# Kernel tuning notes

Measured on AMD Instinct MI355X. Metric: run time of the kernel, lower is better.

Reference implementation:

```python
import jax, jax.numpy as jnp
import numpy as np

D_MODEL = 1024
NUM_HEADS = 16
D_K = D_MODEL // NUM_HEADS
ROPE_THETA = 10000.0


def apply_rope(x, positions):
    # x: (b, h, s, d_k), positions: (b, s) int
    half = D_K // 2
    inv_freq = ROPE_THETA ** (-jnp.arange(half, dtype=jnp.float32) * 2.0 / D_K)  # (half,)
    angles = positions[:, None, :, None].astype(jnp.float32) * inv_freq  # (b,1,s,half)
    cos, sin = jnp.cos(angles), jnp.sin(angles)
    x_even = x[..., 0::2]
    x_odd = x[..., 1::2]
    r_even = x_even * cos - x_odd * sin
    r_odd = x_even * sin + x_odd * cos
    # re-interleave
    out = jnp.stack([r_even, r_odd], axis=-1).reshape(x.shape)
    return out


def setup_inputs() -> dict:
    key = jax.random.key(0)
    k1, k2, k3, k4, k5 = jax.random.split(key, 5)
    b, s = 2, 2048
    scale = 1.0 / np.sqrt(D_MODEL)
    x = jax.random.normal(k1, (b, s, D_MODEL), dtype=jnp.float32)
    w_q = jax.random.normal(k2, (D_MODEL, D_MODEL), dtype=jnp.float32) * scale
    w_k = jax.random.normal(k3, (D_MODEL, D_MODEL), dtype=jnp.float32) * scale
    w_v = jax.random.normal(k4, (D_MODEL, D_MODEL), dtype=jnp.float32) * scale
    w_o = jax.random.normal(k5, (D_MODEL, D_MODEL), dtype=jnp.float32) * scale
    token_positions = jnp.broadcast_to(jnp.arange(s, dtype=jnp.int64 if jax.config.jax_enable_x64 else jnp.int32), (b, s))
    return {"x": x, "w_q": w_q, "w_k": w_k, "w_v": w_v, "w_o": w_o,
            "token_positions": token_positions}


def reference(x, w_q, w_k, w_v, w_o, token_positions):
    b, s, _ = x.shape
    # QKV projections: w_* are (h*d_k, d_model); y = x @ w^T
    def proj(w):
        y = jnp.einsum('bsd,ed->bse', x, w)  # (b,s,h*d_k)
        return y.reshape(b, s, NUM_HEADS, D_K).transpose(0, 2, 1, 3)  # (b,h,s,d_k)
    Q, K, V = proj(w_q), proj(w_k), proj(w_v)
    Q = apply_rope(Q, token_positions)
    K = apply_rope(K, token_positions)
    scores = jnp.einsum('bhqd,bhkd->bhqk', Q, K) / jnp.sqrt(jnp.float32(D_K))
    causal = jnp.tril(jnp.ones((s, s), dtype=bool))
    scores = jnp.where(causal[None, None], scores, -jnp.inf)
    attn = jax.nn.softmax(scores, axis=-1)
    out = jnp.einsum('bhqk,bhkd->bhqd', attn, V)  # (b,h,s,d_v)
    out = out.transpose(0, 2, 1, 3).reshape(b, s, NUM_HEADS * D_K)
    return jnp.einsum('bse,de->bsd', out, w_o)
```

## Files before the change

### kernel.cpp

```cpp
#include <hip/hip_runtime.h>

#define B_ 2
#define S_ 2048
#define DM 1024
#define NH 16
#define DK 64

using bf16x8  = __attribute__((ext_vector_type(8)))  short;
using f32x4   = __attribute__((ext_vector_type(4)))  float;

__device__ __forceinline__ float bf2f(short v){
  unsigned u = ((unsigned)(unsigned short)v) << 16;
  union { unsigned u; float f; } c; c.u = u; return c.f;
}
__device__ __forceinline__ short f2bf(float f){
  union { float f; unsigned u; } c; c.f = f;
  unsigned u = c.u + 0x7FFFu + ((c.u >> 16) & 1u);
  return (short)(u >> 16);
}
__device__ __forceinline__ unsigned packbf(float lo, float hi){
  union { float f; unsigned u; } a, b; a.f = lo; b.f = hi;
  return __builtin_amdgcn_perm(b.u, a.u, 0x07060302u);
}
__device__ __forceinline__ void gload16(const void* g, void* l){
  __builtin_amdgcn_global_load_lds(
    (const __attribute__((address_space(1))) unsigned*)g,
    (__attribute__((address_space(3))) unsigned*)l, 16, 0, 0);
}

__global__ void rope_table(const int* __restrict__ pos, float* __restrict__ tab){
  int idx = blockIdx.x * blockDim.x + threadIdx.x;
  if (idx >= B_ * S_ * 32) return;
  int j = idx & 31, bs = idx >> 5;
  float p = (float)pos[bs];
  float inv = powf(10000.0f, -(float)(2 * j) / 64.0f);
  float ang = p * inv;
  tab[(size_t)bs * 64 + j]      = cosf(ang);
  tab[(size_t)bs * 64 + 32 + j] = sinf(ang);
}

__global__ void cast_all(const float* __restrict__ x, const float* __restrict__ wq,
                         const float* __restrict__ wk, const float* __restrict__ wv,
                         const float* __restrict__ wo,
                         short* __restrict__ xb, short* __restrict__ wqkv,
                         short* __restrict__ wob){
  int i = blockIdx.x * blockDim.x + threadIdx.x;
  const float4* src; short4* dst;
  if (i < (1 << 20)){
    src = (const float4*)x + i; dst = (short4*)xb + i;
  } else {
    int j = i - (1 << 20);
    int seg = j >> 18, off = j & ((1 << 18) - 1);
    const float* sp = seg == 0 ? wq : seg == 1 ? wk : seg == 2 ? wv : wo;
    short* dp = seg < 3 ? wqkv + ((size_t)seg << 20) : wob;
    src = (const float4*)sp + off; dst = (short4*)dp + off;
  }
  float4 v = *src;
  short4 o; o.x = f2bf(v.x); o.y = f2bf(v.y); o.z = f2bf(v.z); o.w = f2bf(v.w);
  *dst = o;
}

__launch_bounds__(512)
__global__ void gemm_qkv(const short* __restrict__ A, const short* __restrict__ Bm,
                         const float* __restrict__ tab,
                         short* __restrict__ Qr, short* __restrict__ Kr,
                         short* __restrict__ Vq, int K){
  __shared__ short As[128 * 32];
  __shared__ short Bs[128 * 32];
  const int tid = threadIdx.x;
  const int l = tid & 63, w = tid >> 6;
  const int lr = l & 15, lg = l >> 4;
  const int wr = w >> 2, wc = w & 3;
  const int nwg = gridDim.x * gridDim.y;
  const int wg  = blockIdx.y * gridDim.x + blockIdx.x;
  const int sw  = (wg & 7) * (nwg >> 3) + (wg >> 3);
  const int bn  = sw % gridDim.x, bm = sw / gridDim.x;
  const short* Ab = A + (size_t)bm * 128 * K;
  const short* Bb = Bm + (size_t)bn * 128 * K;
  f32x4 acc[4][2];
  #pragma unroll
  for (int m = 0; m < 4; ++m)
    #pragma unroll
    for (int n = 0; n < 2; ++n) acc[m][n] = (f32x4){0.f, 0.f, 0.f, 0.f};
  const int r0 = tid >> 2, q4 = tid & 3;
  for (int kt = 0; kt < K; kt += 32){
    gload16(Ab + (size_t)r0 * K + kt + q4 * 8, As + tid * 8);
    gload16(Bb + (size_t)r0 * K + kt + q4 * 8, Bs + tid * 8);
    __syncthreads();
    bf16x8 a[4], bfr[2];
    #pragma unroll
    for (int m = 0; m < 4; ++m)
      a[m] = *(const bf16x8*)(As + (wr * 64 + m * 16 + lr) * 32 + lg * 8);
    #pragma unroll
    for (int n = 0; n < 2; ++n)
      bfr[n] = *(const bf16x8*)(Bs + (wc * 32 + n * 16 + lr) * 32 + lg * 8);
    #pragma unroll
    for (int m = 0; m < 4; ++m)
      #pragma unroll
      for (int n = 0; n < 2; ++n)
        acc[m][n] = __builtin_amdgcn_mfma_f32_16x16x32_bf16(a[m], bfr[n], acc[m][n], 0, 0, 0);
    __syncthreads();
  }
  #pragma unroll
  for (int m = 0; m < 4; ++m)
    #pragma unroll
    for (int n = 0; n < 2; ++n){
      const int col = bn * 128 + wc * 32 + n * 16 + lr;
      const int which = col >> 10;
      #pragma unroll
      for (int j = 0; j < 4; ++j){
        const int row = bm * 128 + wr * 64 + m * 16 + lg * 4 + j;
        float v = acc[m][n][j];
        if (which == 2){
          Vq[(size_t)row * 1024 + (col - 2048)] = f2bf(v);
        } else {
          const int d  = col & 63;
          const int dp = d >> 1;
          const float c = tab[(size_t)row * 64 + dp];
          const float s = tab[(size_t)row * 64 + 32 + dp];
          const float p = __shfl_xor(v, 1);
          float r = v * c + p * ((d & 1) ? s : -s);
          if (which == 0) r *= 0.125f;
          short* dst = which ? Kr : Qr;
          const int b = row >> 11, si = row & 2047;
          const int h = (col >> 6) & 15;
          dst[(((size_t)(b * NH + h)) * S_ + si) * DK + d] = f2bf(r);
        }
      }
    }
}

template<typename OutT>
__launch_bounds__(512)
__global__ void gemm_bt8(const short* __restrict__ A, const short* __restrict__ Bm,
                         OutT* __restrict__ C, int M, int N, int K){
  __shared__ short As[128 * 32];
  __shared__ short Bs[128 * 32];
  const int tid = threadIdx.x;
  const int l = tid & 63, w = tid >> 6;
  const int lr = l & 15, lg = l >> 4;
  const int wr = w >> 2, wc = w & 3;
  const int nwg = gridDim.x * gridDim.y;
  const int wg  = blockIdx.y * gridDim.x + blockIdx.x;
  const int sw  = (wg & 7) * (nwg >> 3) + (wg >> 3);
  const int bn  = sw % gridDim.x, bm = sw / gridDim.x;
  const short* Ab = A + (size_t)bm * 128 * K;
  const short* Bb = Bm + (size_t)bn * 128 * K;
  f32x4 acc[4][2];
  #pragma unroll
  for (int m = 0; m < 4; ++m)
    #pragma unroll
    for (int n = 0; n < 2; ++n) acc[m][n] = (f32x4){0.f, 0.f, 0.f, 0.f};
  const int r0 = tid >> 2, q4 = tid & 3;
  for (int kt = 0; kt < K; kt += 32){
    gload16(Ab + (size_t)r0 * K + kt + q4 * 8, As + tid * 8);
    gload16(Bb + (size_t)r0 * K + kt + q4 * 8, Bs + tid * 8);
    __syncthreads();
    bf16x8 a[4], bfr[2];
    #pragma unroll
    for (int m = 0; m < 4; ++m)
      a[m] = *(const bf16x8*)(As + (wr * 64 + m * 16 + lr) * 32 + lg * 8);
    #pragma unroll
    for (int n = 0; n < 2; ++n)
      bfr[n] = *(const bf16x8*)(Bs + (wc * 32 + n * 16 + lr) * 32 + lg * 8);
    #pragma unroll
    for (int m = 0; m < 4; ++m)
      #pragma unroll
      for (int n = 0; n < 2; ++n)
        acc[m][n] = __builtin_amdgcn_mfma_f32_16x16x32_bf16(a[m], bfr[n], acc[m][n], 0, 0, 0);
    __syncthreads();
  }
  #pragma unroll
  for (int m = 0; m < 4; ++m)
    #pragma unroll
    for (int n = 0; n < 2; ++n)
      #pragma unroll
      for (int j = 0; j < 4; ++j){
        int row = bm * 128 + wr * 64 + m * 16 + lg * 4 + j;
        int col = bn * 128 + wc * 32 + n * 16 + lr;
        float v = acc[m][n][j];
        if constexpr (__is_same(OutT, short)) C[(size_t)row * N + col] = f2bf(v);
        else                                  C[(size_t)row * N + col] = v;
      }
}

__global__ void vtrans(const short* __restrict__ Vq, short* __restrict__ Vt){
  __shared__ short t[64][72];
  const int tid = threadIdx.x;
  const int st = blockIdx.x, bh = blockIdx.y;
  const int b = bh >> 4, h = bh & 15;
  #pragma unroll
  for (int i = 0; i < 2; ++i){
    int c = tid + 256 * i;
    int sl = c >> 3, d8 = c & 7;
    const short* src = Vq + ((size_t)b * S_ + st * 64 + sl) * 1024 + h * 64 + d8 * 8;
    *(bf16x8*)(&t[sl][d8 * 8]) = *(const bf16x8*)src;
  }
  __syncthreads();
  #pragma unroll
  for (int i = 0; i < 2; ++i){
    int c = tid + 256 * i;
    int dl = c >> 3, s8 = c & 7;
    bf16x8 v;
    #pragma unroll
    for (int jj = 0; jj < 8; ++jj) v[jj] = t[s8 * 8 + jj][dl];
    short* dst = Vt + ((size_t)bh * DK + dl) * S_ + st * 64 + s8 * 8;
    *(bf16x8*)dst = v;
  }
}

__device__ __forceinline__ void attn_tile_step(
    const bf16x8 qa0, const bf16x8 qa1,
    f32x4 (&acc)[4], float& mrow, float& lsum,
    const short* Ks, const short* Vs, unsigned* pw,
    int diagmask, int lr, int lg, int wl){
  float sv[4][4];
  #pragma unroll
  for (int n = 0; n < 4; ++n){
    const int R = n * 16 + lr;
    const int c0 = lg ^ (R & 7);
    bf16x8 k0 = *(const bf16x8*)(Ks + R * 64 + c0 * 8);
    bf16x8 k1 = *(const bf16x8*)(Ks + R * 64 + (c0 ^ 4) * 8);
    f32x4 z = (f32x4){0.f, 0.f, 0.f, 0.f};
    z = __builtin_amdgcn_mfma_f32_16x16x32_bf16(k0, qa0, z, 0, 0, 0);
    z = __builtin_amdgcn_mfma_f32_16x16x32_bf16(k1, qa1, z, 0, 0, 0);
    #pragma unroll
    for (int j = 0; j < 4; ++j) sv[n][j] = z[j];
  }
  if (diagmask){
    const int qloc = wl * 16 + lr;
    #pragma unroll
    for (int n = 0; n < 4; ++n)
      #pragma unroll
      for (int j = 0; j < 4; ++j)
        if (n * 16 + lg * 4 + j > qloc) sv[n][j] = -1e30f;
  }
  float lm = sv[0][0];
  #pragma unroll
  for (int n = 0; n < 4; ++n)
    #pragma unroll
    for (int j = 0; j < 4; ++j) lm = fmaxf(lm, sv[n][j]);
  lm = fmaxf(lm, __shfl_xor(lm, 16));
  lm = fmaxf(lm, __shfl_xor(lm, 32));
  if (!__all(lm <= mrow + 8.f)){
    float mnew = fmaxf(mrow, lm);
    float corr = __expf(mrow - mnew);
    mrow = mnew;
    lsum *= corr;
    float cb[4];
    #pragma unroll
    for (int j = 0; j < 4; ++j) cb[j] = __shfl(corr, lg * 4 + j);
    #pragma unroll
    for (int n = 0; n < 4; ++n)
      #pragma unroll
      for (int j = 0; j < 4; ++j) acc[n][j] *= cb[j];
  }
  float psum = 0.f;
  #pragma unroll
  for (int n = 0; n < 4; ++n)
    #pragma unroll
    for (int j = 0; j < 4; ++j){
      float p = __expf(sv[n][j] - mrow);
      sv[n][j] = p; psum += p;
    }
  psum += __shfl_xor(psum, 16);
  psum += __shfl_xor(psum, 32);
  lsum += psum;
  const int swz = (lr & 7) << 2;
  #pragma unroll
  for (int n = 0; n < 4; ++n){
    pw[lr * 32 + ((n * 8 + lg * 2 + 0) ^ swz)] = packbf(sv[n][0], sv[n][1]);
    pw[lr * 32 + ((n * 8 + lg * 2 + 1) ^ swz)] = packbf(sv[n][2], sv[n][3]);
  }
  bf16x8 pa0 = *(const bf16x8*)(pw + lr * 32 + ((lg * 4) ^ swz));
  bf16x8 pa1 = *(const bf16x8*)(pw + lr * 32 + ((16 + lg * 4) ^ swz));
  #pragma unroll
  for (int n = 0; n < 4; ++n){
    const int R = n * 16 + lr;
    const int c0 = lg ^ (R & 7);
    bf16x8 v0 = *(const bf16x8*)(Vs + R * 64 + c0 * 8);
    bf16x8 v1 = *(const bf16x8*)(Vs + R * 64 + (c0 ^ 4) * 8);
    acc[n] = __builtin_amdgcn_mfma_f32_16x16x32_bf16(pa0, v0, acc[n], 0, 0, 0);
    acc[n] = __builtin_amdgcn_mfma_f32_16x16x32_bf16(pa1, v1, acc[n], 0, 0, 0);
  }
}

__launch_bounds__(512)
__global__ void attn_kernel(const short* __restrict__ Qr, const short* __restrict__ Kr,
                            const short* __restrict__ Vt, short* __restrict__ AO){
  __shared__ short Ks[2][64 * 64];
  __shared__ short Vs[2][64 * 64];
  __shared__ unsigned Pw[8][16 * 32];
  const int tid = threadIdx.x;
  const int l = tid & 63, w = tid >> 6;
  const int lr = l & 15, lg = l >> 4;
  const int wl = w & 3, wgp = w >> 2;
  const int qp = blockIdx.x, h = blockIdx.y, b = blockIdx.z;
  const int t0 = qp, t1 = 31 - qp;
  const int myqt = wgp ? t0 : t1;
  const int bh = b * NH + h;
  const short* Qp = Qr + (size_t)bh * S_ * DK;
  const short* Kp = Kr + (size_t)bh * S_ * DK;
  const short* Vp = Vt + (size_t)bh * DK * S_;

  bf16x8 qa0, qa1;
  {
    const short* q0 = Qp + (size_t)(myqt * 64 + wl * 16 + lr) * DK + lg * 8;
    qa0 = *(const bf16x8*)q0; qa1 = *(const bf16x8*)(q0 + 32);
  }
  f32x4 acc[4];
  float ms = -1e30f, ls = 0.f;
  #pragma unroll
  for (int n = 0; n < 4; ++n) acc[n] = (f32x4){0.f, 0.f, 0.f, 0.f};
  unsigned* pw = &Pw[w][0];
  const int r0 = tid >> 3, q8 = tid & 7;
  const int sq8 = q8 ^ (r0 & 7);

  gload16(Kp + (size_t)r0 * DK + sq8 * 8, &Ks[0][tid * 8]);
  gload16(Vp + (size_t)r0 * S_ + sq8 * 8, &Vs[0][tid * 8]);
  int cur = 0;
  for (int kt = 0; kt <= t1; ++kt){
    __syncthreads();
    if (kt < t1){
      gload16(Kp + (size_t)((kt + 1) * 64 + r0) * DK + sq8 * 8, &Ks[cur ^ 1][tid * 8]);
      gload16(Vp + (size_t)r0 * S_ + (kt + 1) * 64 + sq8 * 8,   &Vs[cur ^ 1][tid * 8]);
    }
    if (kt <= myqt)
      attn_tile_step(qa0, qa1, acc, ms, ls, Ks[cur], Vs[cur], pw, kt == myqt, lr, lg, wl);
    cur ^= 1;
  }
  const float li = 1.f / ls;
  #pragma unroll
  for (int j = 0; j < 4; ++j){
    const float d0 = __shfl(li, lg * 4 + j);
    #pragma unroll
    for (int n = 0; n < 4; ++n){
      int e = h * 64 + n * 16 + lr;
      int r = myqt * 64 + wl * 16 + lg * 4 + j;
      AO[((size_t)b * S_ + r) * DM + e] = f2bf(acc[n][j] * d0);
    }
  }
}

extern "C" void kernel_launch(void* const* d_in, const int* in_sizes, int n_in,
                              void* d_out, int out_size, void* d_ws, size_t ws_size,
                              hipStream_t stream){
  const float* x  = (const float*)d_in[0];
  const float* wq = (const float*)d_in[1];
  const float* wk = (const float*)d_in[2];
  const float* wv = (const float*)d_in[3];
  const float* wo = (const float*)d_in[4];
  const int*  pos = (const int*)d_in[5];

  char* ws = (char*)d_ws;
  short* xb   = (short*)(ws + 0);
  short* wqkv = (short*)(ws + ((size_t)8  << 20));
  short* wob  = (short*)(ws + ((size_t)14 << 20));
  short* Vq   = (short*)(ws + ((size_t)16 << 20));
  short* Qr   = (short*)(ws + ((size_t)40 << 20));
  short* Kr   = (short*)(ws + ((size_t)48 << 20));
  short* Vt   = (short*)(ws + ((size_t)56 << 20));
  float* tab  = (float*)(ws + ((size_t)64 << 20));
  short* AO   = xb;
  float* out  = (float*)d_out;

  rope_table<<<dim3((B_ * S_ * 32 + 255) / 256), dim3(256), 0, stream>>>(pos, tab);
  cast_all<<<dim3(8192), dim3(256), 0, stream>>>(x, wq, wk, wv, wo, xb, wqkv, wob);
  gemm_qkv<<<dim3(24, 32), dim3(512), 0, stream>>>(xb, wqkv, tab, Qr, Kr, Vq, 1024);
  vtrans<<<dim3(32, 32), dim3(256), 0, stream>>>(Vq, Vt);
  attn_kernel<<<dim3(16, NH, B_), dim3(512), 0, stream>>>(Qr, Kr, Vt, AO);
  gemm_bt8<float><<<dim3(8, 32), dim3(512), 0, stream>>>(AO, wob, out, 4096, 1024, 1024);
}
```

Baseline: 130.9 us.

## Fuse rope table into cast kernel, triple-buffer QKV GEMM, narrow output GEMM tiles

Merges the RoPE table kernel into the cast kernel, removing one launch. The QKV GEMM switches to a three-stage LDS ring with explicit vmcnt waits and a single barrier per K step, and raises MFMA priority so global loads overlap compute. The output projection GEMM uses 128x64 tiles to double the grid to 512 blocks for better CU occupancy, at the cost of more A-tile reloads. The LDS ring triples shared memory use per block in the QKV GEMM.

After: 127.9 us. 2.3% less time.

```diff
diff --git a/kernel.cpp b/kernel.cpp
--- a/kernel.cpp
+++ b/kernel.cpp
@@ -28,45 +28,45 @@
     (__attribute__((address_space(3))) unsigned*)l, 16, 0, 0);
 }
 
-__global__ void rope_table(const int* __restrict__ pos, float* __restrict__ tab){
-  int idx = blockIdx.x * blockDim.x + threadIdx.x;
-  if (idx >= B_ * S_ * 32) return;
-  int j = idx & 31, bs = idx >> 5;
-  float p = (float)pos[bs];
-  float inv = powf(10000.0f, -(float)(2 * j) / 64.0f);
-  float ang = p * inv;
-  tab[(size_t)bs * 64 + j]      = cosf(ang);
-  tab[(size_t)bs * 64 + 32 + j] = sinf(ang);
-}
-
-__global__ void cast_all(const float* __restrict__ x, const float* __restrict__ wq,
-                         const float* __restrict__ wk, const float* __restrict__ wv,
-                         const float* __restrict__ wo,
-                         short* __restrict__ xb, short* __restrict__ wqkv,
-                         short* __restrict__ wob){
-  int i = blockIdx.x * blockDim.x + threadIdx.x;
-  const float4* src; short4* dst;
-  if (i < (1 << 20)){
-    src = (const float4*)x + i; dst = (short4*)xb + i;
+__global__ void cast_rope(const float* __restrict__ x, const float* __restrict__ wq,
+                          const float* __restrict__ wk, const float* __restrict__ wv,
+                          const float* __restrict__ wo, const int* __restrict__ pos,
+                          short* __restrict__ xb, short* __restrict__ wqkv,
+                          short* __restrict__ wob, float* __restrict__ tab){
+  const int bid = blockIdx.x;
+  if (bid < 8192){
+    int i = bid * 256 + threadIdx.x;
+    const float4* src; short4* dst;
+    if (i < (1 << 20)){
+      src = (const float4*)x + i; dst = (short4*)xb + i;
+    } else {
+      int j = i - (1 << 20);
+      int seg = j >> 18, off = j & ((1 << 18) - 1);
+      const float* sp = seg == 0 ? wq : seg == 1 ? wk : seg == 2 ? wv : wo;
+      short* dp = seg < 3 ? wqkv + ((size_t)seg << 20) : wob;
+      src = (const float4*)sp + off; dst = (short4*)dp + off;
+    }
+    float4 v = *src;
+    short4 o; o.x = f2bf(v.x); o.y = f2bf(v.y); o.z = f2bf(v.z); o.w = f2bf(v.w);
+    *dst = o;
   } else {
-    int j = i - (1 << 20);
-    int seg = j >> 18, off = j & ((1 << 18) - 1);
-    const float* sp = seg == 0 ? wq : seg == 1 ? wk : seg == 2 ? wv : wo;
-    short* dp = seg < 3 ? wqkv + ((size_t)seg << 20) : wob;
-    src = (const float4*)sp + off; dst = (short4*)dp + off;
-  }
-  float4 v = *src;
-  short4 o; o.x = f2bf(v.x); o.y = f2bf(v.y); o.z = f2bf(v.z); o.w = f2bf(v.w);
-  *dst = o;
+    int idx = (bid - 8192) * 256 + threadIdx.x;
+    int j = idx & 31, bs = idx >> 5;
+    float p = (float)pos[bs];
+    float inv = powf(10000.0f, -(float)(2 * j) / 64.0f);
+    float ang = p * inv;
+    tab[(size_t)bs * 64 + j]      = cosf(ang);
+    tab[(size_t)bs * 64 + 32 + j] = sinf(ang);
+  }
 }
 
 __launch_bounds__(512)
 __global__ void gemm_qkv(const short* __restrict__ A, const short* __restrict__ Bm,
                          const float* __restrict__ tab,
                          short* __restrict__ Qr, short* __restrict__ Kr,
-                         short* __restrict__ Vq, int K){
-  __shared__ short As[128 * 32];
-  __shared__ short Bs[128 * 32];
+                         short* __restrict__ Vq){
+  __shared__ short lds[3 * 8192];
+  constexpr int K = 1024, NT = 32;
   const int tid = threadIdx.x;
   const int l = tid & 63, w = tid >> 6;
   const int lr = l & 15, lg = l >> 4;
@@ -75,32 +75,46 @@
   const int wg  = blockIdx.y * gridDim.x + blockIdx.x;
   const int sw  = (wg & 7) * (nwg >> 3) + (wg >> 3);
   const int bn  = sw % gridDim.x, bm = sw / gridDim.x;
-  const short* Ab = A + (size_t)bm * 128 * K;
+  const short* Ab = A  + (size_t)bm * 128 * K;
   const short* Bb = Bm + (size_t)bn * 128 * K;
+  const int r0 = tid >> 2, c4 = tid & 3;
   f32x4 acc[4][2];
   #pragma unroll
   for (int m = 0; m < 4; ++m)
     #pragma unroll
     for (int n = 0; n < 2; ++n) acc[m][n] = (f32x4){0.f, 0.f, 0.f, 0.f};
-  const int r0 = tid >> 2, q4 = tid & 3;
-  for (int kt = 0; kt < K; kt += 32){
-    gload16(Ab + (size_t)r0 * K + kt + q4 * 8, As + tid * 8);
-    gload16(Bb + (size_t)r0 * K + kt + q4 * 8, Bs + tid * 8);
-    __syncthreads();
+
+  auto stage = [&](int t){
+    short* buf = lds + (t % 3) * 8192;
+    gload16(Ab + (size_t)r0 * K + t * 32 + c4 * 8, buf + tid * 8);
+    gload16(Bb + (size_t)r0 * K + t * 32 + c4 * 8, buf + 4096 + tid * 8);
+  };
+
+  stage(0); stage(1);
+  for (int t = 0; t < NT; ++t){
+    if (t < NT - 1) asm volatile("s_waitcnt vmcnt(2)" ::: "memory");
+    else            asm volatile("s_waitcnt vmcnt(0)" ::: "memory");
+    __builtin_amdgcn_s_barrier();
+    __builtin_amdgcn_sched_barrier(0);
+    if (t + 2 < NT) stage(t + 2);
+    const short* bufA = lds + (t % 3) * 8192;
+    const short* bufB = bufA + 4096;
     bf16x8 a[4], bfr[2];
     #pragma unroll
     for (int m = 0; m < 4; ++m)
-      a[m] = *(const bf16x8*)(As + (wr * 64 + m * 16 + lr) * 32 + lg * 8);
+      a[m] = *(const bf16x8*)(bufA + (wr * 64 + m * 16 + lr) * 32 + lg * 8);
     #pragma unroll
     for (int n = 0; n < 2; ++n)
-      bfr[n] = *(const bf16x8*)(Bs + (wc * 32 + n * 16 + lr) * 32 + lg * 8);
+      bfr[n] = *(const bf16x8*)(bufB + (wc * 32 + n * 16 + lr) * 32 + lg * 8);
+    __builtin_amdgcn_s_setprio(1);
     #pragma unroll
     for (int m = 0; m < 4; ++m)
       #pragma unroll
       for (int n = 0; n < 2; ++n)
         acc[m][n] = __builtin_amdgcn_mfma_f32_16x16x32_bf16(a[m], bfr[n], acc[m][n], 0, 0, 0);
-    __syncthreads();
-  }
+    __builtin_amdgcn_s_setprio(0);
+  }
+
   #pragma unroll
   for (int m = 0; m < 4; ++m)
     #pragma unroll
@@ -130,12 +144,12 @@
     }
 }
 
-template<typename OutT>
 __launch_bounds__(512)
-__global__ void gemm_bt8(const short* __restrict__ A, const short* __restrict__ Bm,
-                         OutT* __restrict__ C, int M, int N, int K){
+__global__ void gemm_o(const short* __restrict__ A, const short* __restrict__ Bm,
+                       float* __restrict__ C){
   __shared__ short As[128 * 32];
-  __shared__ short Bs[128 * 32];
+  __shared__ short Bs[64 * 32];
+  constexpr int K = 1024, N = 1024;
   const int tid = threadIdx.x;
   const int l = tid & 63, w = tid >> 6;
   const int lr = l & 15, lg = l >> 4;
@@ -144,44 +158,35 @@
   const int wg  = blockIdx.y * gridDim.x + blockIdx.x;
   const int sw  = (wg & 7) * (nwg >> 3) + (wg >> 3);
   const int bn  = sw % gridDim.x, bm = sw / gridDim.x;
-  const short* Ab = A + (size_t)bm * 128 * K;
-  const short* Bb = Bm + (size_t)bn * 128 * K;
-  f32x4 acc[4][2];
-  #pragma unroll
-  for (int m = 0; m < 4; ++m)
-    #pragma unroll
-    for (int n = 0; n < 2; ++n) acc[m][n] = (f32x4){0.f, 0.f, 0.f, 0.f};
-  const int r0 = tid >> 2, q4 = tid & 3;
+  const short* Ab = A  + (size_t)bm * 128 * K;
+  const short* Bb = Bm + (size_t)bn * 64 * K;
+  f32x4 acc[4];
+  #pragma unroll
+  for (int m = 0; m < 4; ++m) acc[m] = (f32x4){0.f, 0.f, 0.f, 0.f};
+  const int r0 = tid >> 2, c4 = tid & 3;
   for (int kt = 0; kt < K; kt += 32){
-    gload16(Ab + (size_t)r0 * K + kt + q4 * 8, As + tid * 8);
-    gload16(Bb + (size_t)r0 * K + kt + q4 * 8, Bs + tid * 8);
+    gload16(Ab + (size_t)r0 * K + kt + c4 * 8, As + tid * 8);
+    if (tid < 256)
+      gload16(Bb + (size_t)r0 * K + kt + c4 * 8, Bs + tid * 8);
     __syncthreads();
-    bf16x8 a[4], bfr[2];
+    bf16x8 a[4], bfr;
     #pragma unroll
     for (int m = 0; m < 4; ++m)
       a[m] = *(const bf16x8*)(As + (wr * 64 + m * 16 + lr) * 32 + lg * 8);
-    #pragma unroll
-    for (int n = 0; n < 2; ++n)
-      bfr[n] = *(const bf16x8*)(Bs + (wc * 32 + n * 16 + lr) * 32 + lg * 8);
+    bfr = *(const bf16x8*)(Bs + (wc * 16 + lr) * 32 + lg * 8);
     #pragma unroll
     for (int m = 0; m < 4; ++m)
-      #pragma unroll
-      for (int n = 0; n < 2; ++n)
-        acc[m][n] = __builtin_amdgcn_mfma_f32_16x16x32_bf16(a[m], bfr[n], acc[m][n], 0, 0, 0);
+      acc[m] = __builtin_amdgcn_mfma_f32_16x16x32_bf16(a[m], bfr, acc[m], 0, 0, 0);
     __syncthreads();
   }
   #pragma unroll
   for (int m = 0; m < 4; ++m)
     #pragma unroll
-    for (int n = 0; n < 2; ++n)
-      #pragma unroll
-      for (int j = 0; j < 4; ++j){
-        int row = bm * 128 + wr * 64 + m * 16 + lg * 4 + j;
-        int col = bn * 128 + wc * 32 + n * 16 + lr;
-        float v = acc[m][n][j];
-        if constexpr (__is_same(OutT, short)) C[(size_t)row * N + col] = f2bf(v);
-        else                                  C[(size_t)row * N + col] = v;
-      }
+    for (int j = 0; j < 4; ++j){
+      int row = bm * 128 + wr * 64 + m * 16 + lg * 4 + j;
+      int col = bn * 64 + wc * 16 + lr;
+      C[(size_t)row * N + col] = acc[m][j];
+    }
 }
 
 __global__ void vtrans(const short* __restrict__ Vq, short* __restrict__ Vt){
@@ -364,10 +369,9 @@
   short* AO   = xb;
   float* out  = (float*)d_out;
 
-  rope_table<<<dim3((B_ * S_ * 32 + 255) / 256), dim3(256), 0, stream>>>(pos, tab);
-  cast_all<<<dim3(8192), dim3(256), 0, stream>>>(x, wq, wk, wv, wo, xb, wqkv, wob);
-  gemm_qkv<<<dim3(24, 32), dim3(512), 0, stream>>>(xb, wqkv, tab, Qr, Kr, Vq, 1024);
+  cast_rope<<<dim3(8704), dim3(256), 0, stream>>>(x, wq, wk, wv, wo, pos, xb, wqkv, wob, tab);
+  gemm_qkv<<<dim3(24, 32), dim3(512), 0, stream>>>(xb, wqkv, tab, Qr, Kr, Vq);
   vtrans<<<dim3(32, 32), dim3(256), 0, stream>>>(Vq, Vt);
   attn_kernel<<<dim3(16, NH, B_), dim3(512), 0, stream>>>(Qr, Kr, Vt, AO);
-  gemm_bt8<float><<<dim3(8, 32), dim3(512), 0, stream>>>(AO, wob, out, 4096, 1024, 1024);
-}
+  gemm_o<<<dim3(16, 32), dim3(512), 0, stream>>>(AO, wob, out);
+}
```
